# Kernel tuning notes

Measured on AMD Instinct MI355X. Metric: run time of the kernel, lower is better.

The kernel has to match this reference:

```python
import jax, jax.numpy as jnp
import numpy as np

B, S, DIM, H = 2, 2048, 1024, 16
HD = DIM // H  # head dim = 64


def setup_inputs() -> dict:
    key = jax.random.key(0)
    ks = jax.random.split(key, 10)
    scale = 1.0 / np.sqrt(DIM)
    x = jax.random.normal(ks[0], (B, S, DIM), dtype=jnp.float32)
    # per-head projection weights stacked over heads: [H, DIM, HD]
    Wq = jax.random.normal(ks[1], (H, DIM, HD), dtype=jnp.float32) * scale
    bq = jax.random.normal(ks[2], (H, HD), dtype=jnp.float32) * 0.01
    Wk = jax.random.normal(ks[3], (H, DIM, HD), dtype=jnp.float32) * scale
    bk = jax.random.normal(ks[4], (H, HD), dtype=jnp.float32) * 0.01
    Wv = jax.random.normal(ks[5], (H, DIM, HD), dtype=jnp.float32) * scale
    bv = jax.random.normal(ks[6], (H, HD), dtype=jnp.float32) * 0.01
    # output linear: [DIM, DIM]
    Wo = jax.random.normal(ks[7], (DIM, DIM), dtype=jnp.float32) * scale
    bo = jax.random.normal(ks[8], (DIM,), dtype=jnp.float32) * 0.01
    return {"x": x, "Wq": Wq, "bq": bq, "Wk": Wk, "bk": bk,
            "Wv": Wv, "bv": bv, "Wo": Wo, "bo": bo}


def reference(x, Wq, bq, Wk, bk, Wv, bv, Wo, bo):
    # per-head projections: [B, H, S, HD]
    q = jnp.einsum('bsd,hde->bhse', x, Wq) + bq[None, :, None, :]
    k = jnp.einsum('bsd,hde->bhse', x, Wk) + bk[None, :, None, :]
    v = jnp.einsum('bsd,hde->bhse', x, Wv) + bv[None, :, None, :]
    # causal attention scores: [B, H, S, S], scaled by sqrt(head_dim)
    scores = jnp.einsum('bhse,bhte->bhst', q, k) / jnp.sqrt(jnp.float32(HD))
    causal = jnp.tril(jnp.ones((S, S), dtype=bool))
    scores = jnp.where(causal[None, None], scores, -jnp.inf)
    attn = jax.nn.softmax(scores, axis=-1)
    out = jnp.einsum('bhst,bhte->bhse', attn, v)  # [B, H, S, HD]
    # concat heads in order -> [B, S, DIM]
    out = out.transpose(0, 2, 1, 3).reshape(B, S, DIM)
    return out @ Wo + bo
```

## Files before the change

kernel.cpp:

```cpp
#include <hip/hip_runtime.h>

typedef _Float16 half8 __attribute__((ext_vector_type(8)));
typedef _Float16 half4 __attribute__((ext_vector_type(4)));
typedef float f32x4 __attribute__((ext_vector_type(4)));

#define MFMA32(a, b, c) __builtin_amdgcn_mfma_f32_16x16x32_f16((a), (b), (c), 0, 0, 0)
#define MFMA16(a, b, c) __builtin_amdgcn_mfma_f32_16x16x16f16((a), (b), (c), 0, 0, 0)

static constexpr int Bc = 2, Sc = 2048, DIMc = 1024, Hc = 16, HDc = 64;
static constexpr int Mc = Bc * Sc;
static constexpr int NQKV = 3 * DIMc;

__device__ __forceinline__ void gl_lds16(const _Float16* g, _Float16* l) {
  __builtin_amdgcn_global_load_lds(
      (const __attribute__((address_space(1))) void*)g,
      (__attribute__((address_space(3))) void*)l, 16, 0, 0);
}


__global__ __launch_bounds__(256) void k_prep_all(
    const float* __restrict__ x, const float* __restrict__ Wq,
    const float* __restrict__ Wk, const float* __restrict__ Wv,
    const float* __restrict__ Wo, _Float16* __restrict__ xh,
    _Float16* __restrict__ WallT, _Float16* __restrict__ WoT) {
  __shared__ float Ls[64 * 65];
  const int bx = blockIdx.x, tid = threadIdx.x;
  if (bx < 16384) {
    int i = bx * 256 + tid;
    xh[i] = (_Float16)x[i];
    return;
  }
  int b2 = bx - 16384;
  if (b2 < 768) {
    const int dt = b2 & 15, ph = b2 >> 4;
    const int p = ph >> 4, h = ph & 15;
    const float* W = (p == 0) ? Wq : (p == 1) ? Wk : Wv;
    for (int c = tid; c < 4096; c += 256) {
      int dr = c >> 6, e = c & 63;
      Ls[e * 65 + dr] = W[h * 65536 + (dt * 64 + dr) * 64 + e];
    }
    __syncthreads();
    for (int c = tid; c < 4096; c += 256) {
      int e = c >> 6, dr = c & 63;
      WallT[(size_t)(p * 1024 + h * 64 + e) * 1024 + dt * 64 + dr] = (_Float16)Ls[e * 65 + dr];
    }
  } else {
    int b3 = b2 - 768;
    const int dt = b3 & 15, nt = b3 >> 4;
    for (int c = tid; c < 4096; c += 256) {
      int dr = c >> 6, nl = c & 63;
      Ls[nl * 65 + dr] = Wo[(dt * 64 + dr) * 1024 + nt * 64 + nl];
    }
    __syncthreads();
    for (int c = tid; c < 4096; c += 256) {
      int nl = c >> 6, dr = c & 63;
      WoT[(size_t)(nt * 64 + nl) * 1024 + dt * 64 + dr] = (_Float16)Ls[nl * 65 + dr];
    }
  }
}


#define STAGE_AB(buf, kk0)                                                     \
    for (int it = 0; it < 2; ++it) {                                           \
      int idx = it * 256 + tid;                                                \
      int row = idx >> 2, scb = (idx & 3) ^ ((row >> 1) & 3);                  \
      gl_lds16(&A[(size_t)(m0 + row) * DIMc + (kk0) + scb * 8],                \
               &As[buf][(it * 256 + wave * 64) * 8]);                          \
    }                                                                          \
    for (int it = 0; it < 2; ++it) {                                           \
      int idx = it * 256 + tid;                                                \
      int row = idx >> 2, scb = (idx & 3) ^ ((row >> 1) & 3);                  \
      gl_lds16(&Bt[(size_t)(n0 + row) * DIMc + (kk0) + scb * 8],               \
               &Bs[buf][(it * 256 + wave * 64) * 8]);                          \
    }

#define GEMM_CORE()                                                            \
  __shared__ _Float16 As[2][128 * 32];                                         \
  __shared__ _Float16 Bs[2][128 * 32];                                         \
  const int tid = threadIdx.x;                                                 \
  const int lane = tid & 63, wave = tid >> 6;                                  \
  const int quad = lane >> 4, mr = lane & 15;                                  \
  const int sl = quad ^ ((mr >> 1) & 3);                                       \
  const int wm = wave >> 1, wn = wave & 1;                                     \
  f32x4 acc[4][4];                                                             \
  for (int i = 0; i < 4; i++)                                                  \
    for (int j = 0; j < 4; j++) acc[i][j] = f32x4{0.f, 0.f, 0.f, 0.f};         \
  STAGE_AB(0, 0)                                                               \
  for (int k0 = 0; k0 < DIMc; k0 += 32) {                                      \
    const int cur = (k0 >> 5) & 1;                                             \
    if (k0 + 32 < DIMc) {                                                      \
      STAGE_AB(cur ^ 1, k0 + 32)                                               \
      asm volatile("s_waitcnt vmcnt(4)" ::: "memory");                         \
    } else {                                                                   \
      asm volatile("s_waitcnt vmcnt(0)" ::: "memory");                         \
    }                                                                          \
    __builtin_amdgcn_s_barrier();                                              \
    __builtin_amdgcn_sched_barrier(0);                                         \
    half8 af[4], bf[4];                                                        \
    for (int i = 0; i < 4; i++)                                                \
      af[i] = *(const half8*)&As[cur][(wm * 64 + i * 16 + mr) * 32 + sl * 8];  \
    for (int i = 0; i < 4; i++)                                                \
      bf[i] = *(const half8*)&Bs[cur][(wn * 64 + i * 16 + mr) * 32 + sl * 8];  \
    for (int i = 0; i < 4; i++)                                                \
      for (int j = 0; j < 4; j++) acc[i][j] = MFMA32(af[i], bf[j], acc[i][j]); \
    asm volatile("s_waitcnt lgkmcnt(0)" ::: "memory");                         \
    __builtin_amdgcn_s_barrier();                                              \
    __builtin_amdgcn_sched_barrier(0);                                         \
  }

__global__ __launch_bounds__(256, 3) void k_gemm_qkv(
    const _Float16* __restrict__ xh, const _Float16* __restrict__ WallT,
    const float* __restrict__ bq, const float* __restrict__ bk,
    const float* __restrict__ bv, _Float16* __restrict__ qh,
    _Float16* __restrict__ kh, _Float16* __restrict__ vT) {
  const int id = blockIdx.x;
  const bool qkrole = id < 512;
  const _Float16* A;
  const _Float16* Bt;
  int m0, n0;
  if (qkrole) {
    A = xh; Bt = WallT;
    n0 = (id & 15) * 128; m0 = (id >> 4) * 128;
  } else {
    int j = id - 512;
    A = WallT + (size_t)2048 * DIMc; Bt = xh;
    n0 = (j & 31) * 128; m0 = (j >> 5) * 128;
  }
  GEMM_CORE()
  if (qkrole) {
    for (int i = 0; i < 4; i++) {
      for (int j = 0; j < 4; j++) {
        int col = n0 + wn * 64 + j * 16 + mr;
        int p = col >> 10, rem = col & 1023;
        const float* bias = p ? bk : bq;
        _Float16* dst = p ? kh : qh;
        float bb = bias[rem];
        int h = rem >> 6, e = rem & 63;
        for (int r = 0; r < 4; r++) {
          int row = m0 + wm * 64 + i * 16 + quad * 4 + r;
          int b = row >> 11, s = row & 2047;
          dst[(((size_t)(b * Hc + h)) * Sc + s) * HDc + e] = (_Float16)(acc[i][j][r] + bb);
        }
      }
    }
  } else {
    for (int i = 0; i < 4; i++) {
      int rowb = m0 + wm * 64 + i * 16 + quad * 4;
      for (int j = 0; j < 4; j++) {
        int col = n0 + wn * 64 + j * 16 + mr;
        int b = col >> 11, s = col & 2047;
        for (int r = 0; r < 4; r++) {
          int row = rowb + r;
          vT[(size_t)(b * 1024 + row) * Sc + s] = (_Float16)(acc[i][j][r] + bv[row]);
        }
      }
    }
  }
}

__global__ __launch_bounds__(256) void k_gemm_out(
    const _Float16* __restrict__ A, const _Float16* __restrict__ Bt,
    const float* __restrict__ bo, float* __restrict__ out) {
  const int m0 = blockIdx.y * 128, n0 = blockIdx.x * 128;
  GEMM_CORE()
  for (int i = 0; i < 4; i++) {
    for (int j = 0; j < 4; j++) {
      int col = n0 + wn * 64 + j * 16 + mr;
      float bb = bo[col];
      for (int r = 0; r < 4; r++) {
        int row = m0 + wm * 64 + i * 16 + quad * 4 + r;
        out[(size_t)row * DIMc + col] = acc[i][j][r] + bb;
      }
    }
  }
}


__global__ __launch_bounds__(256, 2) void k_attn(
    const _Float16* __restrict__ qg, const _Float16* __restrict__ kg,
    const _Float16* __restrict__ vTg, _Float16* __restrict__ att) {
  const int bid = blockIdx.x;
  const int qt = 31 - (bid >> 5);
  const int bh = bid & 31;
  const int b = bh >> 4, h = bh & 15;
  const int tid = threadIdx.x, w = tid >> 6, lane = tid & 63;
  const int quad = lane >> 4, mr = lane & 15, m7 = mr & 7, m3 = mr & 3;
  const size_t base = (size_t)bh * (Sc * HDc);
  const _Float16* Kg = kg + base;
  const _Float16* Vg = vTg + ((size_t)b * 1024 + h * 64) * Sc;

  __shared__ _Float16 KV[4][2][2][2048];
  __shared__ float Lsh[4][64];

  const int q0 = qt * 64;
  const int ntt = 2 * qt + 2;
  const int myn = (w < ntt) ? ((ntt - 1 - w) >> 2) + 1 : 0;

  const _Float16 qsc = (_Float16)(0.125f * 1.44269504f);
  half8 aq[4][2];
  for (int qf = 0; qf < 4; ++qf)
    for (int c = 0; c < 2; ++c) {
      half8 v = *(const half8*)&qg[base + (size_t)(q0 + qf * 16 + mr) * 64 + c * 32 + quad * 8];
      for (int j = 0; j < 8; ++j) v[j] = v[j] * qsc;
      aq[qf][c] = v;
    }

  f32x4 o[4][4];
  f32x4 ol[4];
  for (int nf = 0; nf < 4; ++nf)
    for (int qf = 0; qf < 4; ++qf) o[nf][qf] = f32x4{0.f, 0.f, 0.f, 0.f};
  for (int qf = 0; qf < 4; ++qf) ol[qf] = f32x4{0.f, 0.f, 0.f, 0.f};
  const half4 ones = {(_Float16)1.f, (_Float16)1.f, (_Float16)1.f, (_Float16)1.f};

#define STAGE32(dst, tt)                                                       \
  {                                                                            \
    const _Float16* ks = Kg + (size_t)(tt) * 2048;                             \
    const _Float16* vs = Vg + (tt) * 32;                                       \
    for (int it = 0; it < 4; ++it) {                                           \
      int idx = it * 64 + lane;                                                \
      int row = idx >> 3, scb = (idx & 7) ^ (row & 7);                         \
      gl_lds16(ks + (size_t)row * 64 + scb * 8, (dst) + it * 512);             \
    }                                                                          \
    for (int it = 0; it < 4; ++it) {                                           \
      int idx = it * 64 + lane;                                                \
      int row = idx >> 2, scb = (idx & 3) ^ (row & 3);                         \
      gl_lds16(vs + (size_t)row * Sc + scb * 8, (dst) + 2048 + it * 512);      \
    }                                                                          \
  }

  if (myn > 0) STAGE32(&KV[w][0][0][0], w)
  asm volatile("s_waitcnt vmcnt(0)" ::: "memory");

  for (int i = 0; i < myn; ++i) {
    const int t = w + 4 * i;
    const _Float16* Kc = &KV[w][i & 1][0][0];
    const _Float16* Vc = &KV[w][i & 1][1][0];
    if (i + 1 < myn) STAGE32(&KV[w][(i + 1) & 1][0][0], t + 4)

    __builtin_amdgcn_s_setprio(1);
    const int dg = (t - 2 * qt) * 32;
    half4 pf[4][2];
    for (int kf = 0; kf < 2; ++kf) {
      const int r0 = (kf * 16 + mr) * 64;
      half8 k0 = *(const half8*)&Kc[r0 + ((quad ^ m7) * 8)];
      half8 k1 = *(const half8*)&Kc[r0 + (((quad ^ 4) ^ m7) * 8)];
      for (int qf = 0; qf < 4; ++qf) {
        f32x4 z = {0.f, 0.f, 0.f, 0.f};
        z = MFMA32(k0, aq[qf][0], z);
        z = MFMA32(k1, aq[qf][1], z);
        half4 pp;
        const int kvr = dg + kf * 16 + quad * 4;
        for (int r = 0; r < 4; ++r) {
          float p = __builtin_amdgcn_exp2f(z[r]);
          if (kvr + r > qf * 16 + mr) p = 0.f;
          pp[r] = (_Float16)p;
        }
        pf[qf][kf] = pp;
      }
    }

    for (int nf = 0; nf < 4; ++nf) {
      const int rb = (nf * 16 + mr) * 32;
      for (int kc = 0; kc < 2; ++kc) {
        int ch = kc * 2 + (quad >> 1);
        half4 vv = *(const half4*)&Vc[rb + ((ch ^ m3) * 8) + (quad & 1) * 4];
        for (int qf = 0; qf < 4; ++qf)
          o[nf][qf] = MFMA16(vv, pf[qf][kc], o[nf][qf]);
      }
    }
    for (int kc = 0; kc < 2; ++kc)
      for (int qf = 0; qf < 4; ++qf) ol[qf] = MFMA16(ones, pf[qf][kc], ol[qf]);
    __builtin_amdgcn_s_setprio(0);

    asm volatile("s_waitcnt vmcnt(0)" ::: "memory");
  }

  float* Osh = (float*)&KV[0][0][0][0];
  for (int nf = 0; nf < 4; ++nf)
    for (int qf = 0; qf < 4; ++qf)
      for (int r = 0; r < 4; ++r)
        Osh[w * 4096 + (nf * 16 + quad * 4 + r) * 64 + qf * 16 + mr] = o[nf][qf][r];
  if (quad == 0)
    for (int qf = 0; qf < 4; ++qf) Lsh[w][qf * 16 + mr] = ol[qf][0];
  __syncthreads();

  const int q = tid & 63, e0 = (tid >> 6) * 16;
  const float linv = 1.0f / (Lsh[0][q] + Lsh[1][q] + Lsh[2][q] + Lsh[3][q]);
  half8 o0, o1;
  for (int e = 0; e < 8; ++e) {
    float s = Osh[(e0 + e) * 64 + q] + Osh[4096 + (e0 + e) * 64 + q] +
              Osh[8192 + (e0 + e) * 64 + q] + Osh[12288 + (e0 + e) * 64 + q];
    o0[e] = (_Float16)(s * linv);
  }
  for (int e = 8; e < 16; ++e) {
    float s = Osh[(e0 + e) * 64 + q] + Osh[4096 + (e0 + e) * 64 + q] +
              Osh[8192 + (e0 + e) * 64 + q] + Osh[12288 + (e0 + e) * 64 + q];
    o1[e - 8] = (_Float16)(s * linv);
  }
  const size_t orow = ((size_t)(b * Sc + q0 + q)) * DIMc + h * 64 + e0;
  *(half8*)&att[orow] = o0;
  *(half8*)&att[orow + 8] = o1;
#undef STAGE32
}


extern "C" void kernel_launch(void* const* d_in, const int* in_sizes, int n_in,
                              void* d_out, int out_size, void* d_ws, size_t ws_size,
                              hipStream_t stream) {
  const float* x  = (const float*)d_in[0];
  const float* Wq = (const float*)d_in[1];
  const float* bq = (const float*)d_in[2];
  const float* Wk = (const float*)d_in[3];
  const float* bk = (const float*)d_in[4];
  const float* Wv = (const float*)d_in[5];
  const float* bv = (const float*)d_in[6];
  const float* Wo = (const float*)d_in[7];
  const float* bo = (const float*)d_in[8];
  float* out = (float*)d_out;

  _Float16* p = (_Float16*)d_ws;
  _Float16* xh    = p; p += (size_t)Mc * DIMc;
  _Float16* WallT = p; p += (size_t)NQKV * DIMc;
  _Float16* WoT   = p; p += (size_t)DIMc * DIMc;
  _Float16* qh    = p; p += (size_t)Bc * Hc * Sc * HDc;
  _Float16* kh    = p; p += (size_t)Bc * Hc * Sc * HDc;
  _Float16* vT    = p; p += (size_t)Bc * Hc * Sc * HDc;
  _Float16* atth  = p;

  k_prep_all<<<16384 + 768 + 256, 256, 0, stream>>>(x, Wq, Wk, Wv, Wo, xh, WallT, WoT);
  k_gemm_qkv<<<768, 256, 0, stream>>>(xh, WallT, bq, bk, bv, qh, kh, vT);
  k_attn<<<1024, 256, 0, stream>>>(qh, kh, vT, atth);
  k_gemm_out<<<dim3(DIMc / 128, Mc / 128), 256, 0, stream>>>(atth, WoT, bo, out);
}
```

Measured before the change: 194.3 us.

## Give each GEMM wave private LDS tiles to drop block barriers; vectorize x conversion

The shared 128x32 A/B tiles are replaced by per-wave private 64x32 double buffers, so each wave stages and consumes only its own rows and the block-wide barriers in the K loop go away. The loop is unrolled by two K steps with vmcnt-based waits. Each wave now reloads data that other waves in the block would otherwise share, raising global/L2 traffic and doubling LDS per block, so occupancy hints drop to 2 blocks per CU. Separately, the fp32-to-fp16 conversion of x now uses float4 loads and half8 stores, with one eighth of the blocks.

```diff
diff --git a/kernel.cpp b/kernel.cpp
--- a/kernel.cpp
+++ b/kernel.cpp
@@ -25,12 +25,19 @@
     _Float16* __restrict__ WallT, _Float16* __restrict__ WoT) {
   __shared__ float Ls[64 * 65];
   const int bx = blockIdx.x, tid = threadIdx.x;
-  if (bx < 16384) {
-    int i = bx * 256 + tid;
-    xh[i] = (_Float16)x[i];
+  if (bx < 2048) {
+    const int i = bx * 256 + tid;
+    const float4* xf = (const float4*)x;
+    float4 a = xf[i * 2], b = xf[i * 2 + 1];
+    half8 hv;
+    hv[0] = (_Float16)a.x; hv[1] = (_Float16)a.y;
+    hv[2] = (_Float16)a.z; hv[3] = (_Float16)a.w;
+    hv[4] = (_Float16)b.x; hv[5] = (_Float16)b.y;
+    hv[6] = (_Float16)b.z; hv[7] = (_Float16)b.w;
+    *(half8*)&xh[(size_t)i * 8] = hv;
     return;
   }
-  int b2 = bx - 16384;
+  int b2 = bx - 2048;
   if (b2 < 768) {
     const int dt = b2 & 15, ph = b2 >> 4;
     const int p = ph >> 4, h = ph & 15;
@@ -60,55 +67,60 @@
 }
 
 
-#define STAGE_AB(buf, kk0)                                                     \
-    for (int it = 0; it < 2; ++it) {                                           \
-      int idx = it * 256 + tid;                                                \
-      int row = idx >> 2, scb = (idx & 3) ^ ((row >> 1) & 3);                  \
-      gl_lds16(&A[(size_t)(m0 + row) * DIMc + (kk0) + scb * 8],                \
-               &As[buf][(it * 256 + wave * 64) * 8]);                          \
-    }                                                                          \
-    for (int it = 0; it < 2; ++it) {                                           \
-      int idx = it * 256 + tid;                                                \
-      int row = idx >> 2, scb = (idx & 3) ^ ((row >> 1) & 3);                  \
-      gl_lds16(&Bt[(size_t)(n0 + row) * DIMc + (kk0) + scb * 8],               \
-               &Bs[buf][(it * 256 + wave * 64) * 8]);                          \
-    }
+#define STAGE_WP(buf, kk0)                                                     \
+  {                                                                            \
+    const int r_ = lane >> 2;                                                  \
+    const int c_ = ((lane & 3) ^ ((r_ >> 1) & 3)) * 8;                         \
+    for (int it = 0; it < 4; ++it)                                             \
+      gl_lds16(&Arow[(size_t)(it * 16 + r_) * DIMc + (kk0) + c_],              \
+               &SH[wave][buf][0][it * 512]);                                   \
+    for (int it = 0; it < 4; ++it)                                             \
+      gl_lds16(&Brow[(size_t)(it * 16 + r_) * DIMc + (kk0) + c_],              \
+               &SH[wave][buf][1][it * 512]);                                   \
+  }
+
+#define COMPUTE_WP(buf)                                                        \
+  {                                                                            \
+    half8 af[4], bf[4];                                                        \
+    for (int i = 0; i < 4; i++)                                                \
+      af[i] = *(const half8*)&SH[wave][buf][0][(i * 16 + mr) * 32 + sl];       \
+    for (int i = 0; i < 4; i++)                                                \
+      bf[i] = *(const half8*)&SH[wave][buf][1][(i * 16 + mr) * 32 + sl];       \
+    for (int i = 0; i < 4; i++)                                                \
+      for (int j = 0; j < 4; j++) acc[i][j] = MFMA32(af[i], bf[j], acc[i][j]); \
+  }
 
 #define GEMM_CORE()                                                            \
-  __shared__ _Float16 As[2][128 * 32];                                         \
-  __shared__ _Float16 Bs[2][128 * 32];                                         \
+  __shared__ _Float16 SH[4][2][2][64 * 32];        \
   const int tid = threadIdx.x;                                                 \
   const int lane = tid & 63, wave = tid >> 6;                                  \
   const int quad = lane >> 4, mr = lane & 15;                                  \
-  const int sl = quad ^ ((mr >> 1) & 3);                                       \
+  const int sl = (quad ^ ((mr >> 1) & 3)) * 8;                                 \
   const int wm = wave >> 1, wn = wave & 1;                                     \
+  const _Float16* Arow = A + (size_t)(m0 + wm * 64) * DIMc;                    \
+  const _Float16* Brow = Bt + (size_t)(n0 + wn * 64) * DIMc;                   \
   f32x4 acc[4][4];                                                             \
   for (int i = 0; i < 4; i++)                                                  \
     for (int j = 0; j < 4; j++) acc[i][j] = f32x4{0.f, 0.f, 0.f, 0.f};         \
-  STAGE_AB(0, 0)                                                               \
-  for (int k0 = 0; k0 < DIMc; k0 += 32) {                                      \
-    const int cur = (k0 >> 5) & 1;                                             \
-    if (k0 + 32 < DIMc) {                                                      \
-      STAGE_AB(cur ^ 1, k0 + 32)                                               \
-      asm volatile("s_waitcnt vmcnt(4)" ::: "memory");                         \
+  STAGE_WP(0, 0)                                                               \
+  for (int k0 = 0; k0 < DIMc; k0 += 64) {                                      \
+    STAGE_WP(1, k0 + 32)                                                       \
+    asm volatile("s_waitcnt vmcnt(8)" ::: "memory");                           \
+    __builtin_amdgcn_sched_barrier(0);                                         \
+    COMPUTE_WP(0)                                                              \
+    __builtin_amdgcn_sched_barrier(0);                                         \
+    if (k0 + 64 < DIMc) {                                                      \
+      STAGE_WP(0, k0 + 64)                                                     \
+      asm volatile("s_waitcnt vmcnt(8)" ::: "memory");                         \
     } else {                                                                   \
       asm volatile("s_waitcnt vmcnt(0)" ::: "memory");                         \
     }                                                                          \
-    __builtin_amdgcn_s_barrier();                                              \
     __builtin_amdgcn_sched_barrier(0);                                         \
-    half8 af[4], bf[4];                                                        \
-    for (int i = 0; i < 4; i++)                                                \
-      af[i] = *(const half8*)&As[cur][(wm * 64 + i * 16 + mr) * 32 + sl * 8];  \
-    for (int i = 0; i < 4; i++)                                                \
-      bf[i] = *(const half8*)&Bs[cur][(wn * 64 + i * 16 + mr) * 32 + sl * 8];  \
-    for (int i = 0; i < 4; i++)                                                \
-      for (int j = 0; j < 4; j++) acc[i][j] = MFMA32(af[i], bf[j], acc[i][j]); \
-    asm volatile("s_waitcnt lgkmcnt(0)" ::: "memory");                         \
-    __builtin_amdgcn_s_barrier();                                              \
+    COMPUTE_WP(1)                                                              \
     __builtin_amdgcn_sched_barrier(0);                                         \
   }
 
-__global__ __launch_bounds__(256, 3) void k_gemm_qkv(
+__global__ __launch_bounds__(256, 2) void k_gemm_qkv(
     const _Float16* __restrict__ xh, const _Float16* __restrict__ WallT,
     const float* __restrict__ bq, const float* __restrict__ bk,
     const float* __restrict__ bv, _Float16* __restrict__ qh,
@@ -158,7 +170,7 @@
   }
 }
 
-__global__ __launch_bounds__(256) void k_gemm_out(
+__global__ __launch_bounds__(256, 2) void k_gemm_out(
     const _Float16* __restrict__ A, const _Float16* __restrict__ Bt,
     const float* __restrict__ bo, float* __restrict__ out) {
   const int m0 = blockIdx.y * 128, n0 = blockIdx.x * 128;
@@ -327,7 +339,7 @@
   _Float16* vT    = p; p += (size_t)Bc * Hc * Sc * HDc;
   _Float16* atth  = p;
 
-  k_prep_all<<<16384 + 768 + 256, 256, 0, stream>>>(x, Wq, Wk, Wv, Wo, xh, WallT, WoT);
+  k_prep_all<<<2048 + 768 + 256, 256, 0, stream>>>(x, Wq, Wk, Wv, Wo, xh, WallT, WoT);
   k_gemm_qkv<<<768, 256, 0, stream>>>(xh, WallT, bq, bk, bv, qh, kh, vT);
   k_attn<<<1024, 256, 0, stream>>>(qh, kh, vT, atth);
   k_gemm_out<<<dim3(DIMc / 128, Mc / 128), 256, 0, stream>>>(atth, WoT, bo, out);
```

New measurement: 187.9 us. 3.3% less time.
